# Optimization experiments

Hardware: AMD Instinct MI355X
Metric: run time of the kernel (lower is better)

Reference implementation:

```python
import jax, jax.numpy as jnp
import numpy as np

WBITS_MAX = 3.0   # 3-bit signed narrow-range weights: levels in [-3, 3]
ABITS_MAX = 15.0  # 4-bit unsigned activations: levels in [0, 15]


def round_ste(x):
    # straight-through estimator for round (Brevitas uses STE)
    return x + jax.lax.stop_gradient(jnp.round(x) - x)


def quant_weight(w):
    # per-tensor symmetric narrow-range 3-bit fake quant (Int weight per-tensor float)
    s = jnp.max(jnp.abs(w)) / WBITS_MAX
    wq = jnp.clip(round_ste(w / s), -WBITS_MAX, WBITS_MAX) * s
    return wq, s


def quant_bias(b, w_scale, in_step):
    # Brevitas BiasQuant: bias scale = input_scale * weight_scale, no clipping (wide int)
    sb = w_scale * in_step  # in_step is shape (1,)
    return round_ste(b / sb) * sb


def quant_relu(x, s):
    # QuantReLU(bit_width=4): relu then unsigned 4-bit fake quant with learned scale s
    step = s / ABITS_MAX
    return jnp.clip(round_ste(jax.nn.relu(x) / step), 0.0, ABITS_MAX) * step


def conv2d(x, w):
    return jax.lax.conv_general_dilated(
        x, w, window_strides=(1, 1), padding='VALID',
        dimension_numbers=('NCHW', 'OIHW', 'NCHW'))


def maxpool2(x):
    return jax.lax.reduce_window(x, -jnp.inf, jax.lax.max,
                                 (1, 1, 2, 2), (1, 1, 2, 2), 'VALID')


def setup_inputs() -> dict:
    key = jax.random.key(0)
    ks = jax.random.split(key, 16)
    d = {}
    d['x'] = jax.random.normal(ks[0], (256, 3, 160, 160), jnp.float32)
    d['w1'] = jax.random.normal(ks[1], (6, 3, 3, 3), jnp.float32) * 0.2
    d['w2'] = jax.random.normal(ks[2], (12, 6, 3, 3), jnp.float32) * 0.2
    d['b2'] = jax.random.normal(ks[3], (12,), jnp.float32) * 0.1
    d['w3'] = jax.random.normal(ks[4], (18, 12, 3, 3), jnp.float32) * 0.2
    d['b3'] = jax.random.normal(ks[5], (18,), jnp.float32) * 0.1
    d['w4'] = jax.random.normal(ks[6], (18, 18, 3, 3), jnp.float32) * 0.2
    d['b4'] = jax.random.normal(ks[7], (18,), jnp.float32) * 0.1
    d['w5'] = jax.random.normal(ks[8], (18, 18, 3, 3), jnp.float32) * 0.2
    d['b5'] = jax.random.normal(ks[9], (18,), jnp.float32) * 0.1
    d['fw1'] = jax.random.normal(ks[10], (120, 162), jnp.float32) * 0.1
    d['fb1'] = jax.random.normal(ks[11], (120,), jnp.float32) * 0.1
    d['fw2'] = jax.random.normal(ks[12], (84, 120), jnp.float32) * 0.1
    d['fb2'] = jax.random.normal(ks[13], (84,), jnp.float32) * 0.1
    d['fw3'] = jax.random.normal(ks[14], (9, 84), jnp.float32) * 0.1
    for i in range(1, 8):
        d[f's{i}'] = jnp.full((1,), 6.0, jnp.float32)  # learned act scales (calibrated init)
    return d


def reference(x, w1, w2, b2, w3, b3, w4, b4, w5, b5,
              fw1, fb1, fw2, fb2, fw3, s1, s2, s3, s4, s5, s6, s7):
    # stage 1 (note: original forward feeds raw x into conv1, bypassing quant_inp)
    q1, _ = quant_weight(w1)
    out = maxpool2(quant_relu(conv2d(x, q1), s1))            # [B,6,79,79]
    # stage 2
    q2, ws2 = quant_weight(w2)
    bq2 = quant_bias(b2, ws2, s1 / ABITS_MAX)
    out = maxpool2(quant_relu(conv2d(out, q2) + bq2[None, :, None, None], s2))  # [B,12,38,38]
    # stage 3
    q3, ws3 = quant_weight(w3)
    bq3 = quant_bias(b3, ws3, s2 / ABITS_MAX)
    out = maxpool2(quant_relu(conv2d(out, q3) + bq3[None, :, None, None], s3))  # [B,18,18,18]
    # stage 4
    q4, ws4 = quant_weight(w4)
    bq4 = quant_bias(b4, ws4, s3 / ABITS_MAX)
    out = maxpool2(quant_relu(conv2d(out, q4) + bq4[None, :, None, None], s4))  # [B,18,8,8]
    # stage 5
    q5, ws5 = quant_weight(w5)
    bq5 = quant_bias(b5, ws5, s4 / ABITS_MAX)
    out = maxpool2(quant_relu(conv2d(out, q5) + bq5[None, :, None, None], s5))  # [B,18,3,3]
    out = out.reshape(out.shape[0], -1)                      # [B,162]
    # fc1
    qf1, fs1 = quant_weight(fw1)
    bqf1 = quant_bias(fb1, fs1, s5 / ABITS_MAX)
    out = quant_relu(out @ qf1.T + bqf1, s6)                 # [B,120]
    # fc2
    qf2, fs2 = quant_weight(fw2)
    bqf2 = quant_bias(fb2, fs2, s6 / ABITS_MAX)
    out = quant_relu(out @ qf2.T + bqf2, s7)                 # [B,84]
    # fc3 (no bias, output not re-quantized: return_quant_tensor=False default path)
    qf3, _ = quant_weight(fw3)
    return out @ qf3.T                                       # [B,9]
```

## Files before the change

### kernel.cpp

```cpp
#include <hip/hip_runtime.h>
#include <hip/hip_bf16.h>
#include <math.h>
#include <type_traits>

constexpr size_t OFF_OUT1B = 0;
constexpr size_t OFF_OUT2B = (size_t)256 * 6 * 79 * 80;
constexpr size_t OFF_A3B   = 0;

template<int CIN, int COUT, int NCO, int HIN, int WSIN,
         int HPOOL, int WPOOL, int WSOUT, int XG, int RB,
         int THREADS, bool HAS_BIAS, bool IN_U8>
__global__ __launch_bounds__(THREADS)
void conv_stage(const void* __restrict__ in_,
                const float* __restrict__ w_raw,
                const float* __restrict__ b_raw,
                const float* __restrict__ s_prev,
                const float* __restrict__ s_act,
                unsigned char* __restrict__ out)
{
    using TIN = typename std::conditional<IN_U8, unsigned char, float>::type;
    constexpr int GROUPS = COUT / NCO;
    constexpr int W4IN   = WSIN / 4;
    constexpr int NW     = COUT * CIN * 9;
    constexpr int STEPS  = 4 * CIN;
    static_assert(NCO * GROUPS == COUT, "NCO divides COUT");
    static_assert(GROUPS * XG * RB <= THREADS, "single compute pass");
    static_assert(4 * XG == WSOUT, "full padded row coverage");
    static_assert(WSIN % 4 == 0, "vec4 loads");

    __shared__ float lw[NW];
    __shared__ float lb[COUT];
    __shared__ float red[THREADS];

    const int r0  = blockIdx.x * RB;
    const int n   = blockIdx.y;
    const int tid = threadIdx.x;

    float mx = 0.0f;
    for (int i = tid; i < NW; i += THREADS) {
        const float v = w_raw[i];
        lw[i] = v;
        mx = fmaxf(mx, fabsf(v));
    }
    if (HAS_BIAS)
        for (int i = tid; i < COUT; i += THREADS) lb[i] = b_raw[i];
    red[tid] = mx;
    __syncthreads();
    for (int s = THREADS / 2; s > 0; s >>= 1) {
        if (tid < s) red[tid] = fmaxf(red[tid], red[tid + s]);
        __syncthreads();
    }
    const float sw_ = red[0] / 3.0f;
    for (int i = tid; i < NW; i += THREADS) {
        float q = rintf(lw[i] / sw_);
        q = fminf(fmaxf(q, -3.0f), 3.0f);
        lw[i] = q * sw_;
    }
    if (HAS_BIAS) {
        const float sb = sw_ * (s_prev[0] / 15.0f);
        for (int i = tid; i < COUT; i += THREADS)
            lb[i] = rintf(lb[i] / sb) * sb;
    }
    __syncthreads();

    const int o = tid;
    if (o >= GROUPS * XG * RB) return;
    const int cog = o % GROUPS;
    const int xg  = (o / GROUPS) % XG;
    const int ry  = o / (GROUPS * XG);
    const int r   = r0 + ry;
    if (r >= HPOOL) return;

    const float step = s_act[0] / 15.0f;
    float step_in = 0.0f;
    if constexpr (IN_U8) step_in = s_prev[0] / 15.0f;

    const int u0 = 2 * xg;
    const int u1 = 2 * xg + 1;
    const int u2 = (2 * xg + 2 < W4IN) ? (2 * xg + 2) : (W4IN - 1);

    const TIN* in   = (const TIN*)in_;
    const TIN* base = in + (size_t)n * CIN * HIN * WSIN + (size_t)(2 * r) * WSIN;

    float acc[NCO][16];
#pragma unroll
    for (int j = 0; j < NCO; ++j)
#pragma unroll
        for (int i = 0; i < 16; ++i) acc[j][i] = 0.0f;

    float4       fbuf[3][3];
    unsigned int ubuf[3][3];
    float        wv[NCO][9];

#define ISSUE_STEP(S)                                                          \
    {                                                                          \
        const TIN* rp = base + (size_t)((S) >> 2) * HIN * WSIN                 \
                             + (size_t)((S) & 3) * WSIN;                       \
        if constexpr (IN_U8) {                                                 \
            ubuf[(S) % 3][0] = *(const unsigned int*)&rp[4 * u0];              \
            ubuf[(S) % 3][1] = *(const unsigned int*)&rp[4 * u1];              \
            ubuf[(S) % 3][2] = *(const unsigned int*)&rp[4 * u2];              \
        } else {                                                               \
            fbuf[(S) % 3][0] = *(const float4*)&rp[4 * u0];                    \
            fbuf[(S) % 3][1] = *(const float4*)&rp[4 * u1];                    \
            fbuf[(S) % 3][2] = *(const float4*)&rp[4 * u2];                    \
        }                                                                      \
    }

    ISSUE_STEP(0);
    ISSUE_STEP(1);

#pragma unroll
    for (int s = 0; s < STEPS; ++s) {
        const int c  = s >> 2;
        const int rr = s & 3;

        if (s + 2 < STEPS) ISSUE_STEP(s + 2);

        if (rr == 0) {
#pragma unroll
            for (int j = 0; j < NCO; ++j)
#pragma unroll
                for (int k = 0; k < 9; ++k)
                    wv[j][k] = lw[((NCO * cog + j) * CIN + c) * 9 + k];
        }

        float row[12];
        if constexpr (IN_U8) {
#pragma unroll
            for (int k = 0; k < 3; ++k) {
                const unsigned int d = ubuf[s % 3][k];
#pragma unroll
                for (int b = 0; b < 4; ++b)
                    row[4 * k + b] = (float)((d >> (8 * b)) & 0xffu) * step_in;
            }
        } else {
            const float* rv = (const float*)fbuf[s % 3];
#pragma unroll
            for (int i = 0; i < 12; ++i) row[i] = rv[i];
        }

        if (rr < 3) {
#pragma unroll
            for (int j = 0; j < NCO; ++j)
#pragma unroll
                for (int kc = 0; kc < 3; ++kc)
#pragma unroll
                    for (int xx = 0; xx < 8; ++xx)
                        acc[j][xx] = fmaf(row[xx + kc], wv[j][rr * 3 + kc], acc[j][xx]);
        }
        if (rr >= 1) {
#pragma unroll
            for (int j = 0; j < NCO; ++j)
#pragma unroll
                for (int kc = 0; kc < 3; ++kc)
#pragma unroll
                    for (int xx = 0; xx < 8; ++xx)
                        acc[j][8 + xx] = fmaf(row[xx + kc], wv[j][(rr - 1) * 3 + kc], acc[j][8 + xx]);
        }
    }
#undef ISSUE_STEP

#pragma unroll
    for (int j = 0; j < NCO; ++j) {
        const int co = NCO * cog + j;
        const float bias = HAS_BIAS ? lb[co] : 0.0f;
        unsigned int pck = 0;
#pragma unroll
        for (int t = 0; t < 4; ++t) {
            float m = fmaxf(fmaxf(acc[j][2 * t], acc[j][2 * t + 1]),
                            fmaxf(acc[j][8 + 2 * t], acc[j][8 + 2 * t + 1]));
            float v = fmaxf(m + bias, 0.0f);
            float q = rintf(v / step);
            q = fminf(fmaxf(q, 0.0f), 15.0f);
            const unsigned int qi = (4 * xg + t < WPOOL) ? (unsigned int)q : 0u;
            pck |= qi << (8 * t);
        }
        *(unsigned int*)&out[(((size_t)n * COUT + co) * HPOOL + r) * WSOUT + 4 * xg] = pck;
    }
}

__device__ __forceinline__ float wave_max(float v) {
#pragma unroll
    for (int off = 32; off > 0; off >>= 1)
        v = fmaxf(v, __shfl_down(v, off));
    return v;
}

__global__ __launch_bounds__(512)
void conv3_stage(const unsigned char* __restrict__ in2,
                 const float* __restrict__ w3, const float* __restrict__ b3,
                 const float* __restrict__ s2, const float* __restrict__ s3,
                 float* __restrict__ a3)
{
    __shared__ float SLf[12 * 20 * 40];
    __shared__ float lw[1944];
    __shared__ float lb[18];
    __shared__ float red[512];

    const int rb  = blockIdx.x;
    const int n   = blockIdx.y;
    const int tid = threadIdx.x;

    float mx = 0.0f;
    for (int i = tid; i < 1944; i += 512) {
        const float v = w3[i];
        lw[i] = v;
        mx = fmaxf(mx, fabsf(v));
    }
    if (tid < 18) lb[tid] = b3[tid];
    red[tid] = mx;

    const float step2 = s2[0] / 15.0f;
    {
        const unsigned char* src = in2 + (size_t)n * 18240;
        for (int d = tid; d < 2400; d += 512) {
            const int c    = d / 200;
            const int rem  = d - c * 200;
            const int lrow = rem / 10;
            const int dw   = rem - lrow * 10;
            const unsigned int u =
                *(const unsigned int*)&src[c * 1520 + (18 * rb + lrow) * 40 + 4 * dw];
            float* q = &SLf[(c * 20 + lrow) * 40 + 4 * dw];
            q[0] = (float)(u & 0xffu) * step2;
            q[1] = (float)((u >> 8) & 0xffu) * step2;
            q[2] = (float)((u >> 16) & 0xffu) * step2;
            q[3] = (float)(u >> 24) * step2;
        }
    }
    __syncthreads();
    for (int s = 256; s > 0; s >>= 1) {
        if (tid < s) red[tid] = fmaxf(red[tid], red[tid + s]);
        __syncthreads();
    }
    const float sw = red[0] / 3.0f;
    for (int i = tid; i < 1944; i += 512) {
        float q = rintf(lw[i] / sw);
        q = fminf(fmaxf(q, -3.0f), 3.0f);
        lw[i] = q * sw;
    }
    if (tid < 18) {
        const float sb = sw * (s2[0] / 15.0f);
        lb[tid] = rintf(lb[tid] / sb) * sb;
    }
    __syncthreads();

    if (tid >= 486) return;
    const int rloc = tid / 54;
    const int rm   = tid - rloc * 54;
    const int co   = rm / 3;
    const int th   = rm - co * 3;
    const int r    = rb * 9 + rloc;

    const float st = s3[0] / 15.0f;

    float acc0[12], acc1[12];
#pragma unroll
    for (int i = 0; i < 12; ++i) { acc0[i] = 0.f; acc1[i] = 0.f; }

    for (int c = 0; c < 12; ++c) {
        float wv[9];
#pragma unroll
        for (int k = 0; k < 9; ++k) wv[k] = lw[(co * 12 + c) * 9 + k];
#pragma unroll
        for (int rr = 0; rr < 4; ++rr) {
            const float* rp = &SLf[(c * 20 + 2 * rloc + rr) * 40 + 12 * th];
            float4 rv[4];
#pragma unroll
            for (int v = 0; v < 4; ++v) rv[v] = *(const float4*)&rp[4 * v];
            const float* row = (const float*)rv;
            if (rr < 3) {
#pragma unroll
                for (int kc = 0; kc < 3; ++kc)
#pragma unroll
                    for (int xx = 0; xx < 12; ++xx)
                        acc0[xx] = fmaf(row[xx + kc], wv[rr * 3 + kc], acc0[xx]);
            }
            if (rr >= 1) {
#pragma unroll
                for (int kc = 0; kc < 3; ++kc)
#pragma unroll
                    for (int xx = 0; xx < 12; ++xx)
                        acc1[xx] = fmaf(row[xx + kc], wv[(rr - 1) * 3 + kc], acc1[xx]);
            }
        }
    }

    const float bias = lb[co];
    float* orow = a3 + (size_t)n * 5832 + (size_t)co * 324 + (size_t)r * 18 + 6 * th;
#pragma unroll
    for (int x = 0; x < 6; ++x) {
        float m = fmaxf(fmaxf(acc0[2 * x], acc0[2 * x + 1]),
                        fmaxf(acc1[2 * x], acc1[2 * x + 1]));
        float v = fmaxf(m + bias, 0.0f);
        float q = rintf(v / st);
        q = fminf(fmaxf(q, 0.0f), 15.0f);
        orow[x] = q * st;
    }
}

__global__ __launch_bounds__(1024)
void tail456(const float* __restrict__ a3in,
             const float* __restrict__ w4, const float* __restrict__ b4,
             const float* __restrict__ w5, const float* __restrict__ b5,
             const float* __restrict__ fw1, const float* __restrict__ fb1,
             const float* __restrict__ fw2, const float* __restrict__ fb2,
             const float* __restrict__ fw3,
             const float* __restrict__ s3, const float* __restrict__ s4,
             const float* __restrict__ s5, const float* __restrict__ s6,
             const float* __restrict__ s7,
             float* __restrict__ out)
{
    __shared__ float A3[5832];
    __shared__ float W4q[2916], W5q[2916];
    __shared__ float B4q[18], B5q[18];
    __shared__ float O4t[64 * 19 + 1];
    __shared__ float A5[162], A6[120], A7[84];
    __shared__ float part[8][120];
    __shared__ float sm[16][5];
    __shared__ float scales[5];

    const int n    = blockIdx.x;
    const int tid  = threadIdx.x;
    const int wid  = tid >> 6;
    const int lane = tid & 63;

    {
        const float4* src = (const float4*)(a3in + (size_t)n * 5832);
        float4* dst = (float4*)A3;
        for (int i = tid; i < 1458; i += 1024) dst[i] = src[i];
    }
    float m4 = 0.f, m5 = 0.f, g1 = 0.f, g2 = 0.f, g3 = 0.f;
    for (int i = tid; i < 2916; i += 1024) { const float v = w4[i]; W4q[i] = v; m4 = fmaxf(m4, fabsf(v)); }
    for (int i = tid; i < 2916; i += 1024) { const float v = w5[i]; W5q[i] = v; m5 = fmaxf(m5, fabsf(v)); }
    {
        const float4* f1 = (const float4*)fw1;
        for (int i = tid; i < 4860; i += 1024) {
            const float4 v = f1[i];
            g1 = fmaxf(g1, fmaxf(fmaxf(fabsf(v.x), fabsf(v.y)), fmaxf(fabsf(v.z), fabsf(v.w))));
        }
        const float4* f2 = (const float4*)fw2;
        for (int i = tid; i < 2520; i += 1024) {
            const float4 v = f2[i];
            g2 = fmaxf(g2, fmaxf(fmaxf(fabsf(v.x), fabsf(v.y)), fmaxf(fabsf(v.z), fabsf(v.w))));
        }
        const float4* f3 = (const float4*)fw3;
        for (int i = tid; i < 189; i += 1024) {
            const float4 v = f3[i];
            g3 = fmaxf(g3, fmaxf(fmaxf(fabsf(v.x), fabsf(v.y)), fmaxf(fabsf(v.z), fabsf(v.w))));
        }
    }
    if (tid < 18) { B4q[tid] = b4[tid]; B5q[tid] = b5[tid]; }
    m4 = wave_max(m4); m5 = wave_max(m5);
    g1 = wave_max(g1); g2 = wave_max(g2); g3 = wave_max(g3);
    if (lane == 0) {
        sm[wid][0] = m4; sm[wid][1] = m5;
        sm[wid][2] = g1; sm[wid][3] = g2; sm[wid][4] = g3;
    }
    __syncthreads();
    if (tid < 5) {
        float v = sm[0][tid];
#pragma unroll
        for (int w = 1; w < 16; ++w) v = fmaxf(v, sm[w][tid]);
        scales[tid] = v / 3.0f;
    }
    __syncthreads();
    const float sw4 = scales[0], sw5 = scales[1];
    const float sf1 = scales[2], sf2 = scales[3], sf3 = scales[4];

    for (int i = tid; i < 2916; i += 1024) { float q = rintf(W4q[i] / sw4); q = fminf(fmaxf(q, -3.f), 3.f); W4q[i] = q * sw4; }
    for (int i = tid; i < 2916; i += 1024) { float q = rintf(W5q[i] / sw5); q = fminf(fmaxf(q, -3.f), 3.f); W5q[i] = q * sw5; }
    if (tid < 18) {
        const float sb4 = sw4 * (s3[0] / 15.0f); B4q[tid] = rintf(B4q[tid] / sb4) * sb4;
        const float sb5 = sw5 * (s4[0] / 15.0f); B5q[tid] = rintf(B5q[tid] / sb5) * sb5;
    }
    __syncthreads();

    {
        const float st = s4[0] / 15.0f;
        for (int o = tid; o < 1152; o += 1024) {
            const int co = o >> 6;
            const int r  = (o >> 3) & 7;
            const int x  = o & 7;
            float a00 = 0.f, a01 = 0.f, a10 = 0.f, a11 = 0.f;
            for (int c = 0; c < 18; ++c) {
                float win[4][4];
#pragma unroll
                for (int rr = 0; rr < 4; ++rr) {
                    const int base = c * 324 + (2 * r + rr) * 18 + 2 * x;
                    *(float2*)&win[rr][0] = *(const float2*)&A3[base];
                    *(float2*)&win[rr][2] = *(const float2*)&A3[base + 2];
                }
                const float* wp = &W4q[(co * 18 + c) * 9];
#pragma unroll
                for (int kr = 0; kr < 3; ++kr)
#pragma unroll
                    for (int kc = 0; kc < 3; ++kc) {
                        const float wvv = wp[kr * 3 + kc];
                        a00 = fmaf(win[kr    ][kc    ], wvv, a00);
                        a01 = fmaf(win[kr    ][kc + 1], wvv, a01);
                        a10 = fmaf(win[kr + 1][kc    ], wvv, a10);
                        a11 = fmaf(win[kr + 1][kc + 1], wvv, a11);
                    }
            }
            float m = fmaxf(fmaxf(a00, a01), fmaxf(a10, a11));
            float v = fmaxf(m + B4q[co], 0.0f);
            float q = rintf(v / st);
            q = fminf(fmaxf(q, 0.0f), 15.0f);
            O4t[(r * 8 + x) * 19 + co] = q * st;
        }
    }
    __syncthreads();

    {
        const float st = s5[0] / 15.0f;
        if (tid < 162) {
            const int co  = tid / 9;
            const int rem = tid - co * 9;
            const int r   = rem / 3;
            const int x   = rem - r * 3;
            float a00 = 0.f, a01 = 0.f, a10 = 0.f, a11 = 0.f;
            for (int c = 0; c < 18; ++c) {
                float win[4][4];
#pragma unroll
                for (int rr = 0; rr < 4; ++rr)
#pragma unroll
                    for (int cc = 0; cc < 4; ++cc)
                        win[rr][cc] = O4t[((2 * r + rr) * 8 + 2 * x + cc) * 19 + c];
                const float* wp = &W5q[(co * 18 + c) * 9];
#pragma unroll
                for (int kr = 0; kr < 3; ++kr)
#pragma unroll
                    for (int kc = 0; kc < 3; ++kc) {
                        const float wvv = wp[kr * 3 + kc];
                        a00 = fmaf(win[kr    ][kc    ], wvv, a00);
                        a01 = fmaf(win[kr    ][kc + 1], wvv, a01);
                        a10 = fmaf(win[kr + 1][kc    ], wvv, a10);
                        a11 = fmaf(win[kr + 1][kc + 1], wvv, a11);
                    }
            }
            float m = fmaxf(fmaxf(a00, a01), fmaxf(a10, a11));
            float v = fmaxf(m + B5q[co], 0.0f);
            float q = rintf(v / st);
            q = fminf(fmaxf(q, 0.0f), 15.0f);
            A5[tid] = q * st;
        }
    }
    __syncthreads();

    if (tid < 960) {
        const int m  = tid % 120;
        const int ch = tid / 120;
        const int k0 = 21 * ch;
        const int k1 = (ch == 7) ? 162 : k0 + 21;
        float p = 0.f;
        const float* wr = fw1 + (size_t)m * 162;
        for (int k = k0; k < k1; ++k) {
            float q = rintf(wr[k] / sf1);
            q = fminf(fmaxf(q, -3.f), 3.f);
            p = fmaf(A5[k], q * sf1, p);
        }
        part[ch][m] = p;
    }
    __syncthreads();
    if (tid < 120) {
        float acc = part[0][tid];
#pragma unroll
        for (int ch = 1; ch < 8; ++ch) acc += part[ch][tid];
        const float sb = sf1 * (s5[0] / 15.0f);
        acc += rintf(fb1[tid] / sb) * sb;
        const float st = s6[0] / 15.0f;
        float q = rintf(fmaxf(acc, 0.0f) / st);
        q = fminf(fmaxf(q, 0.0f), 15.0f);
        A6[tid] = q * st;
    }
    __syncthreads();

    if (tid < 672) {
        const int m  = tid % 84;
        const int ch = tid / 84;
        const int k0 = 15 * ch;
        float p = 0.f;
        const float* wr = fw2 + (size_t)m * 120;
        for (int k = k0; k < k0 + 15; ++k) {
            float q = rintf(wr[k] / sf2);
            q = fminf(fmaxf(q, -3.f), 3.f);
            p = fmaf(A6[k], q * sf2, p);
        }
        part[ch][m] = p;
    }
    __syncthreads();
    if (tid < 84) {
        float acc = part[0][tid];
#pragma unroll
        for (int ch = 1; ch < 8; ++ch) acc += part[ch][tid];
        const float sb = sf2 * (s6[0] / 15.0f);
        acc += rintf(fb2[tid] / sb) * sb;
        const float st = s7[0] / 15.0f;
        float q = rintf(fmaxf(acc, 0.0f) / st);
        q = fminf(fmaxf(q, 0.0f), 15.0f);
        A7[tid] = q * st;
    }
    __syncthreads();

    if (tid < 63) {
        const int m  = tid % 9;
        const int ch = tid / 9;
        const int k0 = 12 * ch;
        float p = 0.f;
        const float* wr = fw3 + (size_t)m * 84;
        for (int k = k0; k < k0 + 12; ++k) {
            float q = rintf(wr[k] / sf3);
            q = fminf(fmaxf(q, -3.f), 3.f);
            p = fmaf(A7[k], q * sf3, p);
        }
        part[ch][m] = p;
    }
    __syncthreads();
    if (tid < 9) {
        float acc = part[0][tid];
#pragma unroll
        for (int ch = 1; ch < 7; ++ch) acc += part[ch][tid];
        out[(size_t)n * 9 + tid] = acc;
    }
}

extern "C" void kernel_launch(void* const* d_in, const int* in_sizes, int n_in,
                              void* d_out, int out_size, void* d_ws, size_t ws_size,
                              hipStream_t stream)
{
    const float* x   = (const float*)d_in[0];
    const float* w1  = (const float*)d_in[1];
    const float* w2  = (const float*)d_in[2];
    const float* b2  = (const float*)d_in[3];
    const float* w3  = (const float*)d_in[4];
    const float* b3  = (const float*)d_in[5];
    const float* w4  = (const float*)d_in[6];
    const float* b4  = (const float*)d_in[7];
    const float* w5  = (const float*)d_in[8];
    const float* b5  = (const float*)d_in[9];
    const float* fw1 = (const float*)d_in[10];
    const float* fb1 = (const float*)d_in[11];
    const float* fw2 = (const float*)d_in[12];
    const float* fb2 = (const float*)d_in[13];
    const float* fw3 = (const float*)d_in[14];
    const float* s1  = (const float*)d_in[15];
    const float* s2  = (const float*)d_in[16];
    const float* s3  = (const float*)d_in[17];
    const float* s4  = (const float*)d_in[18];
    const float* s5  = (const float*)d_in[19];
    const float* s6  = (const float*)d_in[20];
    const float* s7  = (const float*)d_in[21];

    unsigned char* wsb = (unsigned char*)d_ws;
    float* out = (float*)d_out;

    conv_stage<3, 6, 2, 160, 160, 79, 79, 80, 20, 4, 256, false, false>
        <<<dim3(20, 256), 256, 0, stream>>>(x, w1, nullptr, nullptr, s1,
                                            wsb + OFF_OUT1B);

    conv_stage<6, 12, 2, 79, 80, 38, 38, 40, 10, 4, 256, true, true>
        <<<dim3(10, 256), 256, 0, stream>>>(wsb + OFF_OUT1B, w2, b2, s1, s2,
                                            wsb + OFF_OUT2B);

    conv3_stage<<<dim3(2, 256), 512, 0, stream>>>(wsb + OFF_OUT2B, w3, b3, s2, s3,
                                                  (float*)(wsb + OFF_A3B));

    tail456<<<256, 1024, 0, stream>>>((const float*)(wsb + OFF_A3B),
                                      w4, b4, w5, b5,
                                      fw1, fb1, fw2, fb2, fw3,
                                      s3, s4, s5, s6, s7, out);
}
```

Before: 141.8 us.

## Load conv3 input bytes directly from global with register double-buffering

Drops the 38 KB LDS staging of the dequantized conv3 input tile. Each thread now reads its own uint8 rows straight from global memory into registers, prefetches the next channel while computing the current one, and dequantizes in registers. The aim is to cut LDS footprint and the staging pass so more blocks fit per CU and the load overlaps with compute. The cost is redundant global reads, since neighbouring threads and the 18 output channels reread the same bytes, plus higher register pressure from the fully unrolled channel loop.

```diff
diff --git a/kernel.cpp b/kernel.cpp
--- a/kernel.cpp
+++ b/kernel.cpp
@@ -193,7 +193,6 @@
                  const float* __restrict__ s2, const float* __restrict__ s3,
                  float* __restrict__ a3)
 {
-    __shared__ float SLf[12 * 20 * 40];
     __shared__ float lw[1944];
     __shared__ float lb[18];
     __shared__ float red[512];
@@ -210,24 +209,6 @@
     }
     if (tid < 18) lb[tid] = b3[tid];
     red[tid] = mx;
-
-    const float step2 = s2[0] / 15.0f;
-    {
-        const unsigned char* src = in2 + (size_t)n * 18240;
-        for (int d = tid; d < 2400; d += 512) {
-            const int c    = d / 200;
-            const int rem  = d - c * 200;
-            const int lrow = rem / 10;
-            const int dw   = rem - lrow * 10;
-            const unsigned int u =
-                *(const unsigned int*)&src[c * 1520 + (18 * rb + lrow) * 40 + 4 * dw];
-            float* q = &SLf[(c * 20 + lrow) * 40 + 4 * dw];
-            q[0] = (float)(u & 0xffu) * step2;
-            q[1] = (float)((u >> 8) & 0xffu) * step2;
-            q[2] = (float)((u >> 16) & 0xffu) * step2;
-            q[3] = (float)(u >> 24) * step2;
-        }
-    }
     __syncthreads();
     for (int s = 256; s > 0; s >>= 1) {
         if (tid < s) red[tid] = fmaxf(red[tid], red[tid + s]);
@@ -252,23 +233,47 @@
     const int th   = rm - co * 3;
     const int r    = rb * 9 + rloc;
 
-    const float st = s3[0] / 15.0f;
+    const float step2 = s2[0] / 15.0f;
+    const float st    = s3[0] / 15.0f;
+
+    const unsigned char* base = in2 + (size_t)n * 18240 + (size_t)(2 * r) * 40 + 12 * th;
 
     float acc0[12], acc1[12];
 #pragma unroll
     for (int i = 0; i < 12; ++i) { acc0[i] = 0.f; acc1[i] = 0.f; }
 
+    unsigned int ub[2][16];
+
+#define LOADC(C, B)                                                            \
+    {                                                                          \
+        const unsigned char* cp = base + (size_t)(C) * 1520;                   \
+        _Pragma("unroll")                                                      \
+        for (int rr = 0; rr < 4; ++rr)                                         \
+            _Pragma("unroll")                                                  \
+            for (int k = 0; k < 4; ++k)                                        \
+                ub[B][rr * 4 + k] = *(const unsigned int*)&cp[rr * 40 + 4 * k];\
+    }
+
+    LOADC(0, 0);
+
+#pragma unroll
     for (int c = 0; c < 12; ++c) {
+        if (c + 1 < 12) LOADC(c + 1, (c + 1) & 1);
+
         float wv[9];
 #pragma unroll
         for (int k = 0; k < 9; ++k) wv[k] = lw[(co * 12 + c) * 9 + k];
+
 #pragma unroll
         for (int rr = 0; rr < 4; ++rr) {
-            const float* rp = &SLf[(c * 20 + 2 * rloc + rr) * 40 + 12 * th];
-            float4 rv[4];
-#pragma unroll
-            for (int v = 0; v < 4; ++v) rv[v] = *(const float4*)&rp[4 * v];
-            const float* row = (const float*)rv;
+            float row[16];
+#pragma unroll
+            for (int k = 0; k < 4; ++k) {
+                const unsigned int d = ub[c & 1][rr * 4 + k];
+#pragma unroll
+                for (int b = 0; b < 4; ++b)
+                    row[4 * k + b] = (float)((d >> (8 * b)) & 0xffu) * step2;
+            }
             if (rr < 3) {
 #pragma unroll
                 for (int kc = 0; kc < 3; ++kc)
@@ -285,6 +290,7 @@
             }
         }
     }
+#undef LOADC
 
     const float bias = lb[co];
     float* orow = a3 + (size_t)n * 5832 + (size_t)co * 324 + (size_t)r * 18 + 6 * th;
```

New measurement: 141.4 us. Within noise of the previous version (-0.3%).
